# Kernel tuning notes

Measured on AMD Instinct MI355X. Metric: run time of the kernel, lower is better.

## Reference

```python
import jax, jax.numpy as jnp
import numpy as np

EPS = 1e-6
B, N, K = 4, 65536, 16
D_IN, D_OUT, DH = 8, 16, 8  # DH = d_out // 2


def _bn(x, g, b):
    # train-mode BatchNorm2d over (B, N, K) per channel (channels-last here)
    m = jnp.mean(x, axis=(0, 1, 2))
    v = jnp.var(x, axis=(0, 1, 2))
    return (x - m) * jax.lax.rsqrt(v + EPS) * g + b


def _conv(x, w, b):
    # 1x1 Conv2d == per-point linear; x: (B,N,K,Cin), w: (Cout,Cin)
    return jnp.einsum('bnki,oi->bnko', x, w) + b


def _lse(coords, feats, idx, w, b, g, bt):
    # coords: (B,N,3), feats: (B,N,1,D), idx: (B,N,K)
    nbrs = jnp.take_along_axis(coords[:, :, None, :], idx[:, :, :, None], axis=1)  # (B,N,K,3)
    ctr = jnp.broadcast_to(coords[:, :, None, :], nbrs.shape)
    dist = jnp.ones(idx.shape + (1,), dtype=coords.dtype)  # torch path passes idx only -> dist = ones
    enc = jnp.concatenate([ctr, nbrs, ctr - nbrs, dist], axis=-1)  # (B,N,K,10)
    h = jax.nn.relu(_bn(_conv(enc, w, b), g, bt))
    f = jnp.broadcast_to(feats, idx.shape + (feats.shape[-1],))
    return jnp.concatenate([h, f], axis=-1)  # (B,N,K,2*D)


def _pool(x, sw, w, b, g, bt):
    # attentive pooling: softmax over neighbor axis K (axis=2)
    scores = jax.nn.softmax(jnp.einsum('bnki,oi->bnko', x, sw), axis=2)
    agg = jnp.sum(scores * x, axis=2, keepdims=True)  # (B,N,1,C)
    return jax.nn.relu(_bn(_conv(agg, w, b), g, bt))


def setup_inputs() -> dict:
    key = jax.random.key(0)
    ks = jax.random.split(key, 16)
    rn = lambda k, s: (0.1 * jax.random.normal(k, s)).astype(jnp.float32)
    inp = {
        'coords': jax.random.normal(ks[0], (B, N, 3), dtype=jnp.float32),
        'features': jax.random.normal(ks[1], (B, D_IN, N, 1), dtype=jnp.float32),
        'idx': jax.random.randint(ks[2], (B, N, K), 0, N, dtype=jnp.int32),
        # mlp1: d_in -> d_out//2, no bn, LeakyReLU(0.2)
        'w1': rn(ks[3], (DH, D_IN)), 'b1': jnp.zeros((DH,), jnp.float32),
        # lse1 mlp: 10 -> d_out//2, bn + ReLU
        'lse1_w': rn(ks[4], (DH, 10)), 'lse1_b': jnp.zeros((DH,), jnp.float32),
        'lse1_g': jnp.ones((DH,), jnp.float32), 'lse1_bt': jnp.zeros((DH,), jnp.float32),
        # pool1: in d_out -> out d_out//2
        'p1_sw': rn(ks[5], (D_OUT, D_OUT)),
        'p1_w': rn(ks[6], (DH, D_OUT)), 'p1_b': jnp.zeros((DH,), jnp.float32),
        'p1_g': jnp.ones((DH,), jnp.float32), 'p1_bt': jnp.zeros((DH,), jnp.float32),
        # lse2
        'lse2_w': rn(ks[7], (DH, 10)), 'lse2_b': jnp.zeros((DH,), jnp.float32),
        'lse2_g': jnp.ones((DH,), jnp.float32), 'lse2_bt': jnp.zeros((DH,), jnp.float32),
        # pool2: in d_out -> out d_out
        'p2_sw': rn(ks[8], (D_OUT, D_OUT)),
        'p2_w': rn(ks[9], (D_OUT, D_OUT)), 'p2_b': jnp.zeros((D_OUT,), jnp.float32),
        'p2_g': jnp.ones((D_OUT,), jnp.float32), 'p2_bt': jnp.zeros((D_OUT,), jnp.float32),
        # mlp2: d_out -> 2*d_out (no bn/act)
        'w2': rn(ks[10], (2 * D_OUT, D_OUT)), 'b2': jnp.zeros((2 * D_OUT,), jnp.float32),
        # shortcut: d_in -> 2*d_out, bn, no act
        'sc_w': rn(ks[11], (2 * D_OUT, D_IN)), 'sc_b': jnp.zeros((2 * D_OUT,), jnp.float32),
        'sc_g': jnp.ones((2 * D_OUT,), jnp.float32), 'sc_bt': jnp.zeros((2 * D_OUT,), jnp.float32),
    }
    return inp


def reference(coords, features, idx, w1, b1, lse1_w, lse1_b, lse1_g, lse1_bt,
              p1_sw, p1_w, p1_b, p1_g, p1_bt, lse2_w, lse2_b, lse2_g, lse2_bt,
              p2_sw, p2_w, p2_b, p2_g, p2_bt, w2, b2, sc_w, sc_b, sc_g, sc_bt):
    feats = jnp.transpose(features, (0, 2, 3, 1))  # (B,N,1,d_in) channels-last
    x = jax.nn.leaky_relu(_conv(feats, w1, b1), 0.2)           # (B,N,1,DH)
    x = _lse(coords, x, idx, lse1_w, lse1_b, lse1_g, lse1_bt)  # (B,N,K,D_OUT)
    x = _pool(x, p1_sw, p1_w, p1_b, p1_g, p1_bt)               # (B,N,1,DH)
    x = _lse(coords, x, idx, lse2_w, lse2_b, lse2_g, lse2_bt)  # (B,N,K,D_OUT)
    x = _pool(x, p2_sw, p2_w, p2_b, p2_g, p2_bt)               # (B,N,1,D_OUT)
    out = jax.nn.leaky_relu(
        _conv(x, w2, b2) + _bn(_conv(feats, sc_w, sc_b), sc_g, sc_bt), 0.01)
    return jnp.transpose(out, (0, 3, 1, 2))  # (B, 2*d_out, N, 1)
```

## Files before the change

kernel.cpp:

```cpp
#include <hip/hip_runtime.h>

#define NB 4
#define NN 65536
#define NK 16
#define NP (NB * NN)
#define BN_EPS 1e-6f

#define WS_ENC_M   0
#define WS_SC_M    32
#define WS_S_Y2    96
#define WS_SS_Y2   104
#define WS_S_Y4    112
#define WS_SS_Y4   128
#define WS_BN1_SC  160
#define WS_BN1_SH  168
#define WS_BN3_SC  176
#define WS_BN3_SH  184
#define WS_BNSC_SC 192
#define WS_BNSC_SH 224
#define WS_BNP1_SC 256
#define WS_BNP1_SH 264
#define WS_BNP2_SC 272
#define WS_BNP2_SH 288
#define WS_Y2      1024
#define WS_Y4      (1024 + NP * 8)

template <int NCH>
__device__ inline void blockReduceAtomic(float (&v)[NCH], float* __restrict__ dst) {
    __shared__ float red[4][NCH];
    const int lane = threadIdx.x & 63;
    const int wv = threadIdx.x >> 6;
#pragma unroll
    for (int c = 0; c < NCH; c++) {
        float x = v[c];
#pragma unroll
        for (int off = 32; off > 0; off >>= 1) x += __shfl_xor(x, off, 64);
        if (lane == 0) red[wv][c] = x;
    }
    __syncthreads();
    for (int c = threadIdx.x; c < NCH; c += 256)
        atomicAdd(dst + c, red[0][c] + red[1][c] + red[2][c] + red[3][c]);
}

__global__ __launch_bounds__(256) void k_stats1(
    const float* __restrict__ coords, const float* __restrict__ feats,
    const int* __restrict__ idx, float* __restrict__ ws) {
    const int tid = threadIdx.x;
    const int p = blockIdx.x * 256 + tid;
    const int b = p >> 16;
    const int n = p & (NN - 1);

    {
        float accf[44];
        float f[8];
#pragma unroll
        for (int i = 0; i < 8; i++) f[i] = feats[(b * 8 + i) * NN + n];
#pragma unroll
        for (int i = 0; i < 8; i++) accf[i] = f[i];
        int t2 = 8;
#pragma unroll
        for (int i = 0; i < 8; i++)
#pragma unroll
            for (int j = i; j < 8; j++) accf[t2++] = f[i] * f[j];
        blockReduceAtomic<44>(accf, ws + WS_SC_M);
    }

    const float cx = coords[3 * p], cy = coords[3 * p + 1], cz = coords[3 * p + 2];
    const float* cb = coords + b * NN * 3;
    const int4* ip = (const int4*)idx + p * 4;
    float sn0 = 0.f, sn1 = 0.f, sn2 = 0.f;
    float m00 = 0.f, m01 = 0.f, m02 = 0.f, m11 = 0.f, m12 = 0.f, m22 = 0.f;
#pragma unroll
    for (int q = 0; q < 4; q++) {
        int4 v = ip[q];
        int jj[4] = {v.x, v.y, v.z, v.w};
#pragma unroll
        for (int e = 0; e < 4; e++) {
            const int j = jj[e];
            const float nx = cb[3 * j], ny = cb[3 * j + 1], nz = cb[3 * j + 2];
            sn0 += nx; sn1 += ny; sn2 += nz;
            m00 += nx * nx; m01 += nx * ny; m02 += nx * nz;
            m11 += ny * ny; m12 += ny * nz; m22 += nz * nz;
        }
    }
    float acc[27];
    acc[0] = 16.f * cx; acc[1] = 16.f * cy; acc[2] = 16.f * cz;
    acc[3] = sn0; acc[4] = sn1; acc[5] = sn2;
    acc[6] = 16.f * cx * cx; acc[7] = 16.f * cx * cy; acc[8] = 16.f * cx * cz;
    acc[9] = 16.f * cy * cy; acc[10] = 16.f * cy * cz; acc[11] = 16.f * cz * cz;
    acc[12] = cx * sn0; acc[13] = cx * sn1; acc[14] = cx * sn2;
    acc[15] = cy * sn0; acc[16] = cy * sn1; acc[17] = cy * sn2;
    acc[18] = cz * sn0; acc[19] = cz * sn1; acc[20] = cz * sn2;
    acc[21] = m00; acc[22] = m01; acc[23] = m02;
    acc[24] = m11; acc[25] = m12; acc[26] = m22;
    blockReduceAtomic<27>(acc, ws + WS_ENC_M);
}

__global__ void k_fin1(
    const float* __restrict__ lse1_w, const float* __restrict__ lse1_b,
    const float* __restrict__ g1, const float* __restrict__ bt1,
    const float* __restrict__ lse2_w, const float* __restrict__ lse2_b,
    const float* __restrict__ g3, const float* __restrict__ bt3,
    const float* __restrict__ sc_w, const float* __restrict__ sc_b,
    const float* __restrict__ gsc, const float* __restrict__ btsc,
    float* __restrict__ ws) {
    const int t = threadIdx.x;
    if (t < 16) {
        const int c = t & 7;
        const float* w = (t < 8 ? lse1_w : lse2_w) + c * 10;
        const float bb = (t < 8 ? lse1_b : lse2_b)[c];
        float u[6];
        u[0] = w[0] + w[6]; u[1] = w[1] + w[7]; u[2] = w[2] + w[8];
        u[3] = w[3] - w[6]; u[4] = w[4] - w[7]; u[5] = w[5] - w[8];
        const float beta = bb + w[9];
        const float* M = ws + WS_ENC_M;
        float lin = 0.f;
#pragma unroll
        for (int i = 0; i < 6; i++) lin += u[i] * M[i];
        float quad = u[0] * u[0] * M[6] + 2.f * u[0] * u[1] * M[7] + 2.f * u[0] * u[2] * M[8]
                   + u[1] * u[1] * M[9] + 2.f * u[1] * u[2] * M[10] + u[2] * u[2] * M[11];
#pragma unroll
        for (int i = 0; i < 3; i++)
#pragma unroll
            for (int j = 0; j < 3; j++) quad += 2.f * u[i] * u[3 + j] * M[12 + i * 3 + j];
        quad += u[3] * u[3] * M[21] + 2.f * u[3] * u[4] * M[22] + 2.f * u[3] * u[5] * M[23]
              + u[4] * u[4] * M[24] + 2.f * u[4] * u[5] * M[25] + u[5] * u[5] * M[26];
        const float cnt = (float)NP * (float)NK;
        const float sum = lin + cnt * beta;
        const float ss = quad + 2.f * beta * lin + cnt * beta * beta;
        const float m = sum / cnt, v = ss / cnt - m * m;
        const float g = (t < 8 ? g1 : g3)[c], bt = (t < 8 ? bt1 : bt3)[c];
        const float sc = g * rsqrtf(v + BN_EPS);
        if (t < 8) { ws[WS_BN1_SC + c] = sc; ws[WS_BN1_SH + c] = bt - m * sc; }
        else       { ws[WS_BN3_SC + c] = sc; ws[WS_BN3_SH + c] = bt - m * sc; }
    } else if (t < 48) {
        const int c = t - 16;
        const float* w = sc_w + c * 8;
        const float* S = ws + WS_SC_M;
        float lin = 0.f;
#pragma unroll
        for (int i = 0; i < 8; i++) lin += w[i] * S[i];
        float quad = 0.f;
        int t2 = 0;
#pragma unroll
        for (int i = 0; i < 8; i++)
#pragma unroll
            for (int j = i; j < 8; j++) {
                const float mm = S[8 + t2++];
                quad += (i == j ? 1.f : 2.f) * w[i] * w[j] * mm;
            }
        const float cnt = (float)NP;
        const float bb = sc_b[c];
        const float sum = lin + cnt * bb;
        const float ss = quad + 2.f * bb * lin + cnt * bb * bb;
        const float m = sum / cnt, v = ss / cnt - m * m;
        const float sc = gsc[c] * rsqrtf(v + BN_EPS);
        ws[WS_BNSC_SC + c] = sc; ws[WS_BNSC_SH + c] = btsc[c] - m * sc;
    }
}

__global__ __launch_bounds__(256) void k_pool1(
    const float* __restrict__ coords, const float* __restrict__ feats,
    const int* __restrict__ idx,
    const float* __restrict__ w1, const float* __restrict__ b1,
    const float* __restrict__ lse1_w, const float* __restrict__ lse1_b,
    const float* __restrict__ p1_sw, const float* __restrict__ p1_w,
    const float* __restrict__ p1_b, float* __restrict__ ws) {
    __shared__ float lws[80], lbs[8], w1s[64], b1s[8], bnsc[8], bnsh[8],
        sws[64], pws[128], pbs[8];
    const int tid = threadIdx.x;
    for (int i = tid; i < 80; i += 256) lws[i] = lse1_w[i];
    if (tid < 8) {
        lbs[tid] = lse1_b[tid]; b1s[tid] = b1[tid]; pbs[tid] = p1_b[tid];
        bnsc[tid] = ws[WS_BN1_SC + tid]; bnsh[tid] = ws[WS_BN1_SH + tid];
    }
    if (tid < 64) {
        w1s[tid] = w1[tid];
        int o = tid >> 3, i2 = tid & 7;
        sws[tid] = p1_sw[o * 16 + i2];
    }
    if (tid < 128) pws[tid] = p1_w[tid];
    __syncthreads();

    float st[16] = {};
    const int p = blockIdx.x * 256 + tid;
    if (p < NP) {
        const int b = p >> 16;
        const int n = p & (NN - 1);
        float f[8];
#pragma unroll
        for (int i = 0; i < 8; i++) f[i] = feats[(b * 8 + i) * NN + n];
        float x1[8];
#pragma unroll
        for (int j = 0; j < 8; j++) {
            float y = b1s[j];
#pragma unroll
            for (int i = 0; i < 8; i++) y += f[i] * w1s[j * 8 + i];
            x1[j] = y > 0.f ? y : 0.2f * y;
        }
        const float cx = coords[3 * p], cy = coords[3 * p + 1], cz = coords[3 * p + 2];
        const float* cb = coords + b * NN * 3;
        const int4* ip = (const int4*)idx + p * 4;
        int nb[16];
#pragma unroll
        for (int q = 0; q < 4; q++) {
            int4 v = ip[q];
            nb[4 * q] = v.x; nb[4 * q + 1] = v.y; nb[4 * q + 2] = v.z; nb[4 * q + 3] = v.w;
        }
        float l[8] = {}, ac[8] = {};
#pragma unroll
        for (int k = 0; k < 16; k++) {
            const int j = nb[k];
            const float nx = cb[3 * j], ny = cb[3 * j + 1], nz = cb[3 * j + 2];
            const float e6 = cx - nx, e7 = cy - ny, e8 = cz - nz;
            float h[8];
#pragma unroll
            for (int c = 0; c < 8; c++) {
                const float* w = &lws[c * 10];
                float y = lbs[c] + w[9] + cx * w[0] + cy * w[1] + cz * w[2] +
                          nx * w[3] + ny * w[4] + nz * w[5] + e6 * w[6] + e7 * w[7] + e8 * w[8];
                y = y * bnsc[c] + bnsh[c];
                h[c] = y > 0.f ? y : 0.f;
            }
#pragma unroll
            for (int o = 0; o < 8; o++) {
                float s = 0.f;
#pragma unroll
                for (int i = 0; i < 8; i++) s += h[i] * sws[o * 8 + i];
                float e = __expf(s);
                l[o] += e; ac[o] += e * h[o];
            }
        }
        float agg[16];
#pragma unroll
        for (int o = 0; o < 8; o++) agg[o] = ac[o] / l[o];
#pragma unroll
        for (int o = 0; o < 8; o++) agg[8 + o] = x1[o];
#pragma unroll
        for (int c = 0; c < 8; c++) {
            float y = pbs[c];
#pragma unroll
            for (int o = 0; o < 16; o++) y += agg[o] * pws[c * 16 + o];
            ws[WS_Y2 + c * NP + p] = y;
            st[c] = y; st[8 + c] = y * y;
        }
    }
    blockReduceAtomic<16>(st, ws + WS_S_Y2);
}

__global__ void k_fin2(const float* __restrict__ g, const float* __restrict__ bt,
                       float* __restrict__ ws) {
    const int t = threadIdx.x;
    if (t < 8) {
        const float cP = 1.f / (float)NP;
        float m = ws[WS_S_Y2 + t] * cP, v = ws[WS_SS_Y2 + t] * cP - m * m;
        float sc = g[t] * rsqrtf(v + BN_EPS);
        ws[WS_BNP1_SC + t] = sc; ws[WS_BNP1_SH + t] = bt[t] - m * sc;
    }
}

__global__ __launch_bounds__(256) void k_pool2(
    const float* __restrict__ coords, const int* __restrict__ idx,
    const float* __restrict__ lse2_w, const float* __restrict__ lse2_b,
    const float* __restrict__ p2_sw, const float* __restrict__ p2_w,
    const float* __restrict__ p2_b, float* __restrict__ ws) {
    __shared__ float lws[80], lbs[8], bnsc[8], bnsh[8], p1sc[8], p1sh[8],
        sws[64], pws[256], pbs[16];
    const int tid = threadIdx.x;
    for (int i = tid; i < 80; i += 256) lws[i] = lse2_w[i];
    if (tid < 8) {
        lbs[tid] = lse2_b[tid];
        bnsc[tid] = ws[WS_BN3_SC + tid]; bnsh[tid] = ws[WS_BN3_SH + tid];
        p1sc[tid] = ws[WS_BNP1_SC + tid]; p1sh[tid] = ws[WS_BNP1_SH + tid];
    }
    if (tid < 64) {
        int o = tid >> 3, i2 = tid & 7;
        sws[tid] = p2_sw[o * 16 + i2];
    }
    if (tid < 256) pws[tid] = p2_w[tid];
    if (tid < 16) pbs[tid] = p2_b[tid];
    __syncthreads();

    float st[32] = {};
    const int p = blockIdx.x * 256 + tid;
    if (p < NP) {
        const int b = p >> 16;
        float x2[8];
#pragma unroll
        for (int c = 0; c < 8; c++) {
            float y = ws[WS_Y2 + c * NP + p] * p1sc[c] + p1sh[c];
            x2[c] = y > 0.f ? y : 0.f;
        }
        const float cx = coords[3 * p], cy = coords[3 * p + 1], cz = coords[3 * p + 2];
        const float* cb = coords + b * NN * 3;
        const int4* ip = (const int4*)idx + p * 4;
        int nb[16];
#pragma unroll
        for (int q = 0; q < 4; q++) {
            int4 v = ip[q];
            nb[4 * q] = v.x; nb[4 * q + 1] = v.y; nb[4 * q + 2] = v.z; nb[4 * q + 3] = v.w;
        }
        float l[8] = {}, ac[8] = {};
#pragma unroll
        for (int k = 0; k < 16; k++) {
            const int j = nb[k];
            const float nx = cb[3 * j], ny = cb[3 * j + 1], nz = cb[3 * j + 2];
            const float e6 = cx - nx, e7 = cy - ny, e8 = cz - nz;
            float h[8];
#pragma unroll
            for (int c = 0; c < 8; c++) {
                const float* w = &lws[c * 10];
                float y = lbs[c] + w[9] + cx * w[0] + cy * w[1] + cz * w[2] +
                          nx * w[3] + ny * w[4] + nz * w[5] + e6 * w[6] + e7 * w[7] + e8 * w[8];
                y = y * bnsc[c] + bnsh[c];
                h[c] = y > 0.f ? y : 0.f;
            }
#pragma unroll
            for (int o = 0; o < 8; o++) {
                float s = 0.f;
#pragma unroll
                for (int i = 0; i < 8; i++) s += h[i] * sws[o * 8 + i];
                float e = __expf(s);
                l[o] += e; ac[o] += e * h[o];
            }
        }
        float agg[16];
#pragma unroll
        for (int o = 0; o < 8; o++) agg[o] = ac[o] / l[o];
#pragma unroll
        for (int o = 0; o < 8; o++) agg[8 + o] = x2[o];
#pragma unroll
        for (int c = 0; c < 16; c++) {
            float y = pbs[c];
#pragma unroll
            for (int o = 0; o < 16; o++) y += agg[o] * pws[c * 16 + o];
            ws[WS_Y4 + c * NP + p] = y;
            st[c] = y; st[16 + c] = y * y;
        }
    }
    blockReduceAtomic<32>(st, ws + WS_S_Y4);
}

__global__ void k_fin3(const float* __restrict__ g, const float* __restrict__ bt,
                       float* __restrict__ ws) {
    const int t = threadIdx.x;
    if (t < 16) {
        const float cP = 1.f / (float)NP;
        float m = ws[WS_S_Y4 + t] * cP, v = ws[WS_SS_Y4 + t] * cP - m * m;
        float sc = g[t] * rsqrtf(v + BN_EPS);
        ws[WS_BNP2_SC + t] = sc; ws[WS_BNP2_SH + t] = bt[t] - m * sc;
    }
}

__global__ __launch_bounds__(256) void k_final(
    const float* __restrict__ feats, const float* __restrict__ w2,
    const float* __restrict__ b2, const float* __restrict__ sc_w,
    const float* __restrict__ sc_b, const float* __restrict__ ws,
    float* __restrict__ out) {
    __shared__ float w2s[512], b2s[32], scws[256], scbs[32],
        p2sc[16], p2sh[16], scsc[32], scsh[32];
    const int tid = threadIdx.x;
    for (int i = tid; i < 512; i += 256) w2s[i] = w2[i];
    if (tid < 256) scws[tid] = sc_w[tid];
    if (tid < 32) {
        b2s[tid] = b2[tid]; scbs[tid] = sc_b[tid];
        scsc[tid] = ws[WS_BNSC_SC + tid]; scsh[tid] = ws[WS_BNSC_SH + tid];
    }
    if (tid < 16) { p2sc[tid] = ws[WS_BNP2_SC + tid]; p2sh[tid] = ws[WS_BNP2_SH + tid]; }
    __syncthreads();

    const int p = blockIdx.x * 256 + tid;
    if (p >= NP) return;
    const int b = p >> 16;
    const int n = p & (NN - 1);
    float x4[16];
#pragma unroll
    for (int c = 0; c < 16; c++) {
        float y = ws[WS_Y4 + c * NP + p] * p2sc[c] + p2sh[c];
        x4[c] = y > 0.f ? y : 0.f;
    }
    float f[8];
#pragma unroll
    for (int i = 0; i < 8; i++) f[i] = feats[(b * 8 + i) * NN + n];
#pragma unroll
    for (int c = 0; c < 32; c++) {
        float s = scbs[c];
#pragma unroll
        for (int i = 0; i < 8; i++) s += f[i] * scws[c * 8 + i];
        s = s * scsc[c] + scsh[c];
        float m = b2s[c];
#pragma unroll
        for (int o = 0; o < 16; o++) m += x4[o] * w2s[c * 16 + o];
        float v = m + s;
        out[(b * 32 + c) * NN + n] = v > 0.f ? v : 0.01f * v;
    }
}

extern "C" void kernel_launch(void* const* d_in, const int* in_sizes, int n_in,
                              void* d_out, int out_size, void* d_ws, size_t ws_size,
                              hipStream_t stream) {
    (void)in_sizes; (void)n_in; (void)out_size; (void)ws_size;
    const float* coords = (const float*)d_in[0];
    const float* features = (const float*)d_in[1];
    const int* idx = (const int*)d_in[2];
    const float* w1 = (const float*)d_in[3];
    const float* b1 = (const float*)d_in[4];
    const float* lse1_w = (const float*)d_in[5];
    const float* lse1_b = (const float*)d_in[6];
    const float* lse1_g = (const float*)d_in[7];
    const float* lse1_bt = (const float*)d_in[8];
    const float* p1_sw = (const float*)d_in[9];
    const float* p1_w = (const float*)d_in[10];
    const float* p1_b = (const float*)d_in[11];
    const float* p1_g = (const float*)d_in[12];
    const float* p1_bt = (const float*)d_in[13];
    const float* lse2_w = (const float*)d_in[14];
    const float* lse2_b = (const float*)d_in[15];
    const float* lse2_g = (const float*)d_in[16];
    const float* lse2_bt = (const float*)d_in[17];
    const float* p2_sw = (const float*)d_in[18];
    const float* p2_w = (const float*)d_in[19];
    const float* p2_b = (const float*)d_in[20];
    const float* p2_g = (const float*)d_in[21];
    const float* p2_bt = (const float*)d_in[22];
    const float* w2 = (const float*)d_in[23];
    const float* b2 = (const float*)d_in[24];
    const float* sc_w = (const float*)d_in[25];
    const float* sc_b = (const float*)d_in[26];
    const float* sc_g = (const float*)d_in[27];
    const float* sc_bt = (const float*)d_in[28];
    float* ws = (float*)d_ws;
    float* out = (float*)d_out;

    hipMemsetAsync(ws, 0, 144 * sizeof(float), stream);
    k_stats1<<<NP / 256, 256, 0, stream>>>(coords, features, idx, ws);
    k_fin1<<<1, 64, 0, stream>>>(lse1_w, lse1_b, lse1_g, lse1_bt,
                                 lse2_w, lse2_b, lse2_g, lse2_bt,
                                 sc_w, sc_b, sc_g, sc_bt, ws);
    k_pool1<<<NP / 256, 256, 0, stream>>>(coords, features, idx, w1, b1, lse1_w,
                                          lse1_b, p1_sw, p1_w, p1_b, ws);
    k_fin2<<<1, 64, 0, stream>>>(p1_g, p1_bt, ws);
    k_pool2<<<NP / 256, 256, 0, stream>>>(coords, idx, lse2_w, lse2_b, p2_sw,
                                          p2_w, p2_b, ws);
    k_fin3<<<1, 64, 0, stream>>>(p2_g, p2_bt, ws);
    k_final<<<NP / 256, 256, 0, stream>>>(features, w2, b2, sc_w, sc_b, ws, out);
}
```

Measured before the change: 352.9 us.

## Pad coords to float4 scratch, fold BN finalize kernels into consumers, precompute LSE affine

Adds a prep pass that repacks coords into a float4 array, stored temporarily in the output buffer, so each neighbor gather is one 16-byte load instead of three scalar loads. The three single-block finalize kernels are removed; each consumer kernel now computes its BN scale and shift in its prologue, which cuts launches and serialization points. The LSE conv and BN are folded into per-channel affine coefficients split into a center term and a neighbor term, so the per-neighbor math drops to 3 FMAs per channel. Occupancy hints are added to the pool kernels. Reusing the output buffer as scratch relies on k_final overwriting it afterward.

After: 640.9 us. +81.6%, slower.

```diff
diff --git a/kernel.cpp b/kernel.cpp
--- a/kernel.cpp
+++ b/kernel.cpp
@@ -12,16 +12,6 @@
 #define WS_SS_Y2   104
 #define WS_S_Y4    112
 #define WS_SS_Y4   128
-#define WS_BN1_SC  160
-#define WS_BN1_SH  168
-#define WS_BN3_SC  176
-#define WS_BN3_SH  184
-#define WS_BNSC_SC 192
-#define WS_BNSC_SH 224
-#define WS_BNP1_SC 256
-#define WS_BNP1_SH 264
-#define WS_BNP2_SC 272
-#define WS_BNP2_SH 288
 #define WS_Y2      1024
 #define WS_Y4      (1024 + NP * 8)
 
@@ -42,31 +32,59 @@
         atomicAdd(dst + c, red[0][c] + red[1][c] + red[2][c] + red[3][c]);
 }
 
-__global__ __launch_bounds__(256) void k_stats1(
+__device__ inline void bn_from_enc(const float* __restrict__ M, const float* __restrict__ w,
+                                   float b, float g, float bt, float& sc, float& sh) {
+    float u[6];
+    u[0] = w[0] + w[6]; u[1] = w[1] + w[7]; u[2] = w[2] + w[8];
+    u[3] = w[3] - w[6]; u[4] = w[4] - w[7]; u[5] = w[5] - w[8];
+    const float beta = b + w[9];
+    float lin = 0.f;
+#pragma unroll
+    for (int i = 0; i < 6; i++) lin += u[i] * M[i];
+    float quad = u[0] * u[0] * M[6] + 2.f * u[0] * u[1] * M[7] + 2.f * u[0] * u[2] * M[8]
+               + u[1] * u[1] * M[9] + 2.f * u[1] * u[2] * M[10] + u[2] * u[2] * M[11];
+#pragma unroll
+    for (int i = 0; i < 3; i++)
+#pragma unroll
+        for (int j = 0; j < 3; j++) quad += 2.f * u[i] * u[3 + j] * M[12 + i * 3 + j];
+    quad += u[3] * u[3] * M[21] + 2.f * u[3] * u[4] * M[22] + 2.f * u[3] * u[5] * M[23]
+          + u[4] * u[4] * M[24] + 2.f * u[4] * u[5] * M[25] + u[5] * u[5] * M[26];
+    const float cnt = (float)NP * (float)NK;
+    const float sum = lin + cnt * beta;
+    const float ss = quad + 2.f * beta * lin + cnt * beta * beta;
+    const float m = sum / cnt, v = ss / cnt - m * m;
+    sc = g * rsqrtf(v + BN_EPS);
+    sh = bt - m * sc;
+}
+
+__global__ __launch_bounds__(256) void k_prep(
     const float* __restrict__ coords, const float* __restrict__ feats,
-    const int* __restrict__ idx, float* __restrict__ ws) {
+    float4* __restrict__ c4, float* __restrict__ ws) {
     const int tid = threadIdx.x;
     const int p = blockIdx.x * 256 + tid;
     const int b = p >> 16;
     const int n = p & (NN - 1);
-
-    {
-        float accf[44];
-        float f[8];
-#pragma unroll
-        for (int i = 0; i < 8; i++) f[i] = feats[(b * 8 + i) * NN + n];
-#pragma unroll
-        for (int i = 0; i < 8; i++) accf[i] = f[i];
-        int t2 = 8;
-#pragma unroll
-        for (int i = 0; i < 8; i++)
-#pragma unroll
-            for (int j = i; j < 8; j++) accf[t2++] = f[i] * f[j];
-        blockReduceAtomic<44>(accf, ws + WS_SC_M);
-    }
-
-    const float cx = coords[3 * p], cy = coords[3 * p + 1], cz = coords[3 * p + 2];
-    const float* cb = coords + b * NN * 3;
+    c4[p] = make_float4(coords[3 * p], coords[3 * p + 1], coords[3 * p + 2], 0.f);
+    float accf[44];
+    float f[8];
+#pragma unroll
+    for (int i = 0; i < 8; i++) f[i] = feats[(b * 8 + i) * NN + n];
+#pragma unroll
+    for (int i = 0; i < 8; i++) accf[i] = f[i];
+    int t2 = 8;
+#pragma unroll
+    for (int i = 0; i < 8; i++)
+#pragma unroll
+        for (int j = i; j < 8; j++) accf[t2++] = f[i] * f[j];
+    blockReduceAtomic<44>(accf, ws + WS_SC_M);
+}
+
+__global__ __launch_bounds__(256) void k_stats(
+    const float4* __restrict__ c4, const int* __restrict__ idx, float* __restrict__ ws) {
+    const int tid = threadIdx.x;
+    const int p = blockIdx.x * 256 + tid;
+    const int boff = (p >> 16) << 16;
+    const float4 me = c4[p];
     const int4* ip = (const int4*)idx + p * 4;
     float sn0 = 0.f, sn1 = 0.f, sn2 = 0.f;
     float m00 = 0.f, m01 = 0.f, m02 = 0.f, m11 = 0.f, m12 = 0.f, m22 = 0.f;
@@ -76,65 +94,214 @@
         int jj[4] = {v.x, v.y, v.z, v.w};
 #pragma unroll
         for (int e = 0; e < 4; e++) {
-            const int j = jj[e];
-            const float nx = cb[3 * j], ny = cb[3 * j + 1], nz = cb[3 * j + 2];
-            sn0 += nx; sn1 += ny; sn2 += nz;
-            m00 += nx * nx; m01 += nx * ny; m02 += nx * nz;
-            m11 += ny * ny; m12 += ny * nz; m22 += nz * nz;
+            const float4 nn = c4[boff + jj[e]];
+            sn0 += nn.x; sn1 += nn.y; sn2 += nn.z;
+            m00 += nn.x * nn.x; m01 += nn.x * nn.y; m02 += nn.x * nn.z;
+            m11 += nn.y * nn.y; m12 += nn.y * nn.z; m22 += nn.z * nn.z;
         }
     }
     float acc[27];
-    acc[0] = 16.f * cx; acc[1] = 16.f * cy; acc[2] = 16.f * cz;
+    acc[0] = 16.f * me.x; acc[1] = 16.f * me.y; acc[2] = 16.f * me.z;
     acc[3] = sn0; acc[4] = sn1; acc[5] = sn2;
-    acc[6] = 16.f * cx * cx; acc[7] = 16.f * cx * cy; acc[8] = 16.f * cx * cz;
-    acc[9] = 16.f * cy * cy; acc[10] = 16.f * cy * cz; acc[11] = 16.f * cz * cz;
-    acc[12] = cx * sn0; acc[13] = cx * sn1; acc[14] = cx * sn2;
-    acc[15] = cy * sn0; acc[16] = cy * sn1; acc[17] = cy * sn2;
-    acc[18] = cz * sn0; acc[19] = cz * sn1; acc[20] = cz * sn2;
+    acc[6] = 16.f * me.x * me.x; acc[7] = 16.f * me.x * me.y; acc[8] = 16.f * me.x * me.z;
+    acc[9] = 16.f * me.y * me.y; acc[10] = 16.f * me.y * me.z; acc[11] = 16.f * me.z * me.z;
+    acc[12] = me.x * sn0; acc[13] = me.x * sn1; acc[14] = me.x * sn2;
+    acc[15] = me.y * sn0; acc[16] = me.y * sn1; acc[17] = me.y * sn2;
+    acc[18] = me.z * sn0; acc[19] = me.z * sn1; acc[20] = me.z * sn2;
     acc[21] = m00; acc[22] = m01; acc[23] = m02;
     acc[24] = m11; acc[25] = m12; acc[26] = m22;
     blockReduceAtomic<27>(acc, ws + WS_ENC_M);
 }
 
-__global__ void k_fin1(
+__global__ __launch_bounds__(256, 4) void k_pool1(
+    const float4* __restrict__ c4, const float* __restrict__ feats,
+    const int* __restrict__ idx,
+    const float* __restrict__ w1, const float* __restrict__ b1,
     const float* __restrict__ lse1_w, const float* __restrict__ lse1_b,
-    const float* __restrict__ g1, const float* __restrict__ bt1,
+    const float* __restrict__ lse1_g, const float* __restrict__ lse1_bt,
+    const float* __restrict__ p1_sw, const float* __restrict__ p1_w,
+    const float* __restrict__ p1_b, float* __restrict__ ws) {
+    __shared__ float an[24], dc3[24], dcon[8], sws[64], pws[128], pbs[8], w1s[64], b1s[8];
+    const int tid = threadIdx.x;
+    if (tid < 8) {
+        const int c = tid;
+        const float* w = lse1_w + c * 10;
+        float sc, sh;
+        bn_from_enc(ws + WS_ENC_M, w, lse1_b[c], lse1_g[c], lse1_bt[c], sc, sh);
+#pragma unroll
+        for (int i = 0; i < 3; i++) {
+            an[c * 3 + i] = sc * (w[3 + i] - w[6 + i]);
+            dc3[c * 3 + i] = sc * (w[i] + w[6 + i]);
+        }
+        dcon[c] = sc * (lse1_b[c] + w[9]) + sh;
+        b1s[c] = b1[c]; pbs[c] = p1_b[c];
+    }
+    if (tid < 64) {
+        w1s[tid] = w1[tid];
+        sws[tid] = p1_sw[(tid >> 3) * 16 + (tid & 7)];
+    }
+    if (tid < 128) pws[tid] = p1_w[tid];
+    __syncthreads();
+
+    const int p = blockIdx.x * 256 + tid;
+    const int b = p >> 16;
+    const int n = p & (NN - 1);
+    const int boff = b << 16;
+    const float4 me = c4[p];
+    float d[8];
+#pragma unroll
+    for (int c = 0; c < 8; c++)
+        d[c] = dc3[c * 3] * me.x + dc3[c * 3 + 1] * me.y + dc3[c * 3 + 2] * me.z + dcon[c];
+    const int4* ip = (const int4*)idx + p * 4;
+    float l[8] = {}, ac[8] = {};
+#pragma unroll
+    for (int q = 0; q < 4; q++) {
+        int4 v = ip[q];
+        int jj[4] = {v.x, v.y, v.z, v.w};
+#pragma unroll
+        for (int e = 0; e < 4; e++) {
+            const float4 nn = c4[boff + jj[e]];
+            float h[8];
+#pragma unroll
+            for (int c = 0; c < 8; c++) {
+                float y = an[c * 3] * nn.x + an[c * 3 + 1] * nn.y + an[c * 3 + 2] * nn.z + d[c];
+                h[c] = y > 0.f ? y : 0.f;
+            }
+#pragma unroll
+            for (int o = 0; o < 8; o++) {
+                float s = 0.f;
+#pragma unroll
+                for (int i = 0; i < 8; i++) s += h[i] * sws[o * 8 + i];
+                float e2 = __expf(s);
+                l[o] += e2; ac[o] += e2 * h[o];
+            }
+        }
+    }
+    float f[8];
+#pragma unroll
+    for (int i = 0; i < 8; i++) f[i] = feats[(b * 8 + i) * NN + n];
+    float agg[16];
+#pragma unroll
+    for (int o = 0; o < 8; o++) agg[o] = ac[o] / l[o];
+#pragma unroll
+    for (int j = 0; j < 8; j++) {
+        float y = b1s[j];
+#pragma unroll
+        for (int i = 0; i < 8; i++) y += f[i] * w1s[j * 8 + i];
+        agg[8 + j] = y > 0.f ? y : 0.2f * y;
+    }
+    float st[16];
+#pragma unroll
+    for (int c = 0; c < 8; c++) {
+        float y = pbs[c];
+#pragma unroll
+        for (int o = 0; o < 16; o++) y += agg[o] * pws[c * 16 + o];
+        ws[WS_Y2 + c * NP + p] = y;
+        st[c] = y; st[8 + c] = y * y;
+    }
+    blockReduceAtomic<16>(st, ws + WS_S_Y2);
+}
+
+__global__ __launch_bounds__(256, 4) void k_pool2(
+    const float4* __restrict__ c4, const int* __restrict__ idx,
     const float* __restrict__ lse2_w, const float* __restrict__ lse2_b,
-    const float* __restrict__ g3, const float* __restrict__ bt3,
-    const float* __restrict__ sc_w, const float* __restrict__ sc_b,
-    const float* __restrict__ gsc, const float* __restrict__ btsc,
-    float* __restrict__ ws) {
-    const int t = threadIdx.x;
-    if (t < 16) {
-        const int c = t & 7;
-        const float* w = (t < 8 ? lse1_w : lse2_w) + c * 10;
-        const float bb = (t < 8 ? lse1_b : lse2_b)[c];
-        float u[6];
-        u[0] = w[0] + w[6]; u[1] = w[1] + w[7]; u[2] = w[2] + w[8];
-        u[3] = w[3] - w[6]; u[4] = w[4] - w[7]; u[5] = w[5] - w[8];
-        const float beta = bb + w[9];
-        const float* M = ws + WS_ENC_M;
-        float lin = 0.f;
-#pragma unroll
-        for (int i = 0; i < 6; i++) lin += u[i] * M[i];
-        float quad = u[0] * u[0] * M[6] + 2.f * u[0] * u[1] * M[7] + 2.f * u[0] * u[2] * M[8]
-                   + u[1] * u[1] * M[9] + 2.f * u[1] * u[2] * M[10] + u[2] * u[2] * M[11];
-#pragma unroll
-        for (int i = 0; i < 3; i++)
-#pragma unroll
-            for (int j = 0; j < 3; j++) quad += 2.f * u[i] * u[3 + j] * M[12 + i * 3 + j];
-        quad += u[3] * u[3] * M[21] + 2.f * u[3] * u[4] * M[22] + 2.f * u[3] * u[5] * M[23]
-              + u[4] * u[4] * M[24] + 2.f * u[4] * u[5] * M[25] + u[5] * u[5] * M[26];
-        const float cnt = (float)NP * (float)NK;
-        const float sum = lin + cnt * beta;
-        const float ss = quad + 2.f * beta * lin + cnt * beta * beta;
-        const float m = sum / cnt, v = ss / cnt - m * m;
-        const float g = (t < 8 ? g1 : g3)[c], bt = (t < 8 ? bt1 : bt3)[c];
-        const float sc = g * rsqrtf(v + BN_EPS);
-        if (t < 8) { ws[WS_BN1_SC + c] = sc; ws[WS_BN1_SH + c] = bt - m * sc; }
-        else       { ws[WS_BN3_SC + c] = sc; ws[WS_BN3_SH + c] = bt - m * sc; }
-    } else if (t < 48) {
-        const int c = t - 16;
+    const float* __restrict__ lse2_g, const float* __restrict__ lse2_bt,
+    const float* __restrict__ p1_g, const float* __restrict__ p1_bt,
+    const float* __restrict__ p2_sw, const float* __restrict__ p2_w,
+    const float* __restrict__ p2_b, float* __restrict__ ws) {
+    __shared__ float an[24], dc3[24], dcon[8], p1sc[8], p1sh[8],
+        sws[64], pws[256], pbs[16];
+    const int tid = threadIdx.x;
+    if (tid < 8) {
+        const int c = tid;
+        const float* w = lse2_w + c * 10;
+        float sc, sh;
+        bn_from_enc(ws + WS_ENC_M, w, lse2_b[c], lse2_g[c], lse2_bt[c], sc, sh);
+#pragma unroll
+        for (int i = 0; i < 3; i++) {
+            an[c * 3 + i] = sc * (w[3 + i] - w[6 + i]);
+            dc3[c * 3 + i] = sc * (w[i] + w[6 + i]);
+        }
+        dcon[c] = sc * (lse2_b[c] + w[9]) + sh;
+    } else if (tid < 16) {
+        const int c = tid - 8;
+        const float cP = 1.f / (float)NP;
+        float m = ws[WS_S_Y2 + c] * cP, v = ws[WS_SS_Y2 + c] * cP - m * m;
+        float sc = p1_g[c] * rsqrtf(v + BN_EPS);
+        p1sc[c] = sc; p1sh[c] = p1_bt[c] - m * sc;
+    }
+    if (tid < 64) sws[tid] = p2_sw[(tid >> 3) * 16 + (tid & 7)];
+    if (tid < 256) pws[tid] = p2_w[tid];
+    if (tid < 16) pbs[tid] = p2_b[tid];
+    __syncthreads();
+
+    const int p = blockIdx.x * 256 + tid;
+    const int boff = (p >> 16) << 16;
+    const float4 me = c4[p];
+    float d[8];
+#pragma unroll
+    for (int c = 0; c < 8; c++)
+        d[c] = dc3[c * 3] * me.x + dc3[c * 3 + 1] * me.y + dc3[c * 3 + 2] * me.z + dcon[c];
+    const int4* ip = (const int4*)idx + p * 4;
+    float l[8] = {}, ac[8] = {};
+#pragma unroll
+    for (int q = 0; q < 4; q++) {
+        int4 v = ip[q];
+        int jj[4] = {v.x, v.y, v.z, v.w};
+#pragma unroll
+        for (int e = 0; e < 4; e++) {
+            const float4 nn = c4[boff + jj[e]];
+            float h[8];
+#pragma unroll
+            for (int c = 0; c < 8; c++) {
+                float y = an[c * 3] * nn.x + an[c * 3 + 1] * nn.y + an[c * 3 + 2] * nn.z + d[c];
+                h[c] = y > 0.f ? y : 0.f;
+            }
+#pragma unroll
+            for (int o = 0; o < 8; o++) {
+                float s = 0.f;
+#pragma unroll
+                for (int i = 0; i < 8; i++) s += h[i] * sws[o * 8 + i];
+                float e2 = __expf(s);
+                l[o] += e2; ac[o] += e2 * h[o];
+            }
+        }
+    }
+    float agg[16];
+#pragma unroll
+    for (int o = 0; o < 8; o++) agg[o] = ac[o] / l[o];
+#pragma unroll
+    for (int c = 0; c < 8; c++) {
+        float y = ws[WS_Y2 + c * NP + p] * p1sc[c] + p1sh[c];
+        agg[8 + c] = y > 0.f ? y : 0.f;
+    }
+    float st[32];
+#pragma unroll
+    for (int c = 0; c < 16; c++) {
+        float y = pbs[c];
+#pragma unroll
+        for (int o = 0; o < 16; o++) y += agg[o] * pws[c * 16 + o];
+        ws[WS_Y4 + c * NP + p] = y;
+        st[c] = y; st[16 + c] = y * y;
+    }
+    blockReduceAtomic<32>(st, ws + WS_S_Y4);
+}
+
+__global__ __launch_bounds__(256) void k_final(
+    const float* __restrict__ feats, const float* __restrict__ w2,
+    const float* __restrict__ b2, const float* __restrict__ sc_w,
+    const float* __restrict__ sc_b, const float* __restrict__ p2_g,
+    const float* __restrict__ p2_bt, const float* __restrict__ sc_g,
+    const float* __restrict__ sc_bt, const float* __restrict__ ws,
+    float* __restrict__ out) {
+    __shared__ float w2s[512], b2s[32], scws[256], scbs[32],
+        p2sc[16], p2sh[16], scsc[32], scsh[32];
+    const int tid = threadIdx.x;
+    for (int i = tid; i < 512; i += 256) w2s[i] = w2[i];
+    if (tid < 256) scws[tid] = sc_w[tid];
+    if (tid < 32) {
+        b2s[tid] = b2[tid]; scbs[tid] = sc_b[tid];
+        const int c = tid;
         const float* w = sc_w + c * 8;
         const float* S = ws + WS_SC_M;
         float lin = 0.f;
@@ -154,223 +321,19 @@
         const float sum = lin + cnt * bb;
         const float ss = quad + 2.f * bb * lin + cnt * bb * bb;
         const float m = sum / cnt, v = ss / cnt - m * m;
-        const float sc = gsc[c] * rsqrtf(v + BN_EPS);
-        ws[WS_BNSC_SC + c] = sc; ws[WS_BNSC_SH + c] = btsc[c] - m * sc;
-    }
-}
-
-__global__ __launch_bounds__(256) void k_pool1(
-    const float* __restrict__ coords, const float* __restrict__ feats,
-    const int* __restrict__ idx,
-    const float* __restrict__ w1, const float* __restrict__ b1,
-    const float* __restrict__ lse1_w, const float* __restrict__ lse1_b,
-    const float* __restrict__ p1_sw, const float* __restrict__ p1_w,
-    const float* __restrict__ p1_b, float* __restrict__ ws) {
-    __shared__ float lws[80], lbs[8], w1s[64], b1s[8], bnsc[8], bnsh[8],
-        sws[64], pws[128], pbs[8];
-    const int tid = threadIdx.x;
-    for (int i = tid; i < 80; i += 256) lws[i] = lse1_w[i];
-    if (tid < 8) {
-        lbs[tid] = lse1_b[tid]; b1s[tid] = b1[tid]; pbs[tid] = p1_b[tid];
-        bnsc[tid] = ws[WS_BN1_SC + tid]; bnsh[tid] = ws[WS_BN1_SH + tid];
-    }
-    if (tid < 64) {
-        w1s[tid] = w1[tid];
-        int o = tid >> 3, i2 = tid & 7;
-        sws[tid] = p1_sw[o * 16 + i2];
-    }
-    if (tid < 128) pws[tid] = p1_w[tid];
+        const float sc = sc_g[c] * rsqrtf(v + BN_EPS);
+        scsc[c] = sc; scsh[c] = sc_bt[c] - m * sc;
+    }
+    if (tid < 16) {
+        const int c = tid;
+        const float cP = 1.f / (float)NP;
+        float m = ws[WS_S_Y4 + c] * cP, v = ws[WS_SS_Y4 + c] * cP - m * m;
+        float sc = p2_g[c] * rsqrtf(v + BN_EPS);
+        p2sc[c] = sc; p2sh[c] = p2_bt[c] - m * sc;
+    }
     __syncthreads();
 
-    float st[16] = {};
     const int p = blockIdx.x * 256 + tid;
-    if (p < NP) {
-        const int b = p >> 16;
-        const int n = p & (NN - 1);
-        float f[8];
-#pragma unroll
-        for (int i = 0; i < 8; i++) f[i] = feats[(b * 8 + i) * NN + n];
-        float x1[8];
-#pragma unroll
-        for (int j = 0; j < 8; j++) {
-            float y = b1s[j];
-#pragma unroll
-            for (int i = 0; i < 8; i++) y += f[i] * w1s[j * 8 + i];
-            x1[j] = y > 0.f ? y : 0.2f * y;
-        }
-        const float cx = coords[3 * p], cy = coords[3 * p + 1], cz = coords[3 * p + 2];
-        const float* cb = coords + b * NN * 3;
-        const int4* ip = (const int4*)idx + p * 4;
-        int nb[16];
-#pragma unroll
-        for (int q = 0; q < 4; q++) {
-            int4 v = ip[q];
-            nb[4 * q] = v.x; nb[4 * q + 1] = v.y; nb[4 * q + 2] = v.z; nb[4 * q + 3] = v.w;
-        }
-        float l[8] = {}, ac[8] = {};
-#pragma unroll
-        for (int k = 0; k < 16; k++) {
-            const int j = nb[k];
-            const float nx = cb[3 * j], ny = cb[3 * j + 1], nz = cb[3 * j + 2];
-            const float e6 = cx - nx, e7 = cy - ny, e8 = cz - nz;
-            float h[8];
-#pragma unroll
-            for (int c = 0; c < 8; c++) {
-                const float* w = &lws[c * 10];
-                float y = lbs[c] + w[9] + cx * w[0] + cy * w[1] + cz * w[2] +
-                          nx * w[3] + ny * w[4] + nz * w[5] + e6 * w[6] + e7 * w[7] + e8 * w[8];
-                y = y * bnsc[c] + bnsh[c];
-                h[c] = y > 0.f ? y : 0.f;
-            }
-#pragma unroll
-            for (int o = 0; o < 8; o++) {
-                float s = 0.f;
-#pragma unroll
-                for (int i = 0; i < 8; i++) s += h[i] * sws[o * 8 + i];
-                float e = __expf(s);
-                l[o] += e; ac[o] += e * h[o];
-            }
-        }
-        float agg[16];
-#pragma unroll
-        for (int o = 0; o < 8; o++) agg[o] = ac[o] / l[o];
-#pragma unroll
-        for (int o = 0; o < 8; o++) agg[8 + o] = x1[o];
-#pragma unroll
-        for (int c = 0; c < 8; c++) {
-            float y = pbs[c];
-#pragma unroll
-            for (int o = 0; o < 16; o++) y += agg[o] * pws[c * 16 + o];
-            ws[WS_Y2 + c * NP + p] = y;
-            st[c] = y; st[8 + c] = y * y;
-        }
-    }
-    blockReduceAtomic<16>(st, ws + WS_S_Y2);
-}
-
-__global__ void k_fin2(const float* __restrict__ g, const float* __restrict__ bt,
-                       float* __restrict__ ws) {
-    const int t = threadIdx.x;
-    if (t < 8) {
-        const float cP = 1.f / (float)NP;
-        float m = ws[WS_S_Y2 + t] * cP, v = ws[WS_SS_Y2 + t] * cP - m * m;
-        float sc = g[t] * rsqrtf(v + BN_EPS);
-        ws[WS_BNP1_SC + t] = sc; ws[WS_BNP1_SH + t] = bt[t] - m * sc;
-    }
-}
-
-__global__ __launch_bounds__(256) void k_pool2(
-    const float* __restrict__ coords, const int* __restrict__ idx,
-    const float* __restrict__ lse2_w, const float* __restrict__ lse2_b,
-    const float* __restrict__ p2_sw, const float* __restrict__ p2_w,
-    const float* __restrict__ p2_b, float* __restrict__ ws) {
-    __shared__ float lws[80], lbs[8], bnsc[8], bnsh[8], p1sc[8], p1sh[8],
-        sws[64], pws[256], pbs[16];
-    const int tid = threadIdx.x;
-    for (int i = tid; i < 80; i += 256) lws[i] = lse2_w[i];
-    if (tid < 8) {
-        lbs[tid] = lse2_b[tid];
-        bnsc[tid] = ws[WS_BN3_SC + tid]; bnsh[tid] = ws[WS_BN3_SH + tid];
-        p1sc[tid] = ws[WS_BNP1_SC + tid]; p1sh[tid] = ws[WS_BNP1_SH + tid];
-    }
-    if (tid < 64) {
-        int o = tid >> 3, i2 = tid & 7;
-        sws[tid] = p2_sw[o * 16 + i2];
-    }
-    if (tid < 256) pws[tid] = p2_w[tid];
-    if (tid < 16) pbs[tid] = p2_b[tid];
-    __syncthreads();
-
-    float st[32] = {};
-    const int p = blockIdx.x * 256 + tid;
-    if (p < NP) {
-        const int b = p >> 16;
-        float x2[8];
-#pragma unroll
-        for (int c = 0; c < 8; c++) {
-            float y = ws[WS_Y2 + c * NP + p] * p1sc[c] + p1sh[c];
-            x2[c] = y > 0.f ? y : 0.f;
-        }
-        const float cx = coords[3 * p], cy = coords[3 * p + 1], cz = coords[3 * p + 2];
-        const float* cb = coords + b * NN * 3;
-        const int4* ip = (const int4*)idx + p * 4;
-        int nb[16];
-#pragma unroll
-        for (int q = 0; q < 4; q++) {
-            int4 v = ip[q];
-            nb[4 * q] = v.x; nb[4 * q + 1] = v.y; nb[4 * q + 2] = v.z; nb[4 * q + 3] = v.w;
-        }
-        float l[8] = {}, ac[8] = {};
-#pragma unroll
-        for (int k = 0; k < 16; k++) {
-            const int j = nb[k];
-            const float nx = cb[3 * j], ny = cb[3 * j + 1], nz = cb[3 * j + 2];
-            const float e6 = cx - nx, e7 = cy - ny, e8 = cz - nz;
-            float h[8];
-#pragma unroll
-            for (int c = 0; c < 8; c++) {
-                const float* w = &lws[c * 10];
-                float y = lbs[c] + w[9] + cx * w[0] + cy * w[1] + cz * w[2] +
-                          nx * w[3] + ny * w[4] + nz * w[5] + e6 * w[6] + e7 * w[7] + e8 * w[8];
-                y = y * bnsc[c] + bnsh[c];
-                h[c] = y > 0.f ? y : 0.f;
-            }
-#pragma unroll
-            for (int o = 0; o < 8; o++) {
-                float s = 0.f;
-#pragma unroll
-                for (int i = 0; i < 8; i++) s += h[i] * sws[o * 8 + i];
-                float e = __expf(s);
-                l[o] += e; ac[o] += e * h[o];
-            }
-        }
-        float agg[16];
-#pragma unroll
-        for (int o = 0; o < 8; o++) agg[o] = ac[o] / l[o];
-#pragma unroll
-        for (int o = 0; o < 8; o++) agg[8 + o] = x2[o];
-#pragma unroll
-        for (int c = 0; c < 16; c++) {
-            float y = pbs[c];
-#pragma unroll
-            for (int o = 0; o < 16; o++) y += agg[o] * pws[c * 16 + o];
-            ws[WS_Y4 + c * NP + p] = y;
-            st[c] = y; st[16 + c] = y * y;
-        }
-    }
-    blockReduceAtomic<32>(st, ws + WS_S_Y4);
-}
-
-__global__ void k_fin3(const float* __restrict__ g, const float* __restrict__ bt,
-                       float* __restrict__ ws) {
-    const int t = threadIdx.x;
-    if (t < 16) {
-        const float cP = 1.f / (float)NP;
-        float m = ws[WS_S_Y4 + t] * cP, v = ws[WS_SS_Y4 + t] * cP - m * m;
-        float sc = g[t] * rsqrtf(v + BN_EPS);
-        ws[WS_BNP2_SC + t] = sc; ws[WS_BNP2_SH + t] = bt[t] - m * sc;
-    }
-}
-
-__global__ __launch_bounds__(256) void k_final(
-    const float* __restrict__ feats, const float* __restrict__ w2,
-    const float* __restrict__ b2, const float* __restrict__ sc_w,
-    const float* __restrict__ sc_b, const float* __restrict__ ws,
-    float* __restrict__ out) {
-    __shared__ float w2s[512], b2s[32], scws[256], scbs[32],
-        p2sc[16], p2sh[16], scsc[32], scsh[32];
-    const int tid = threadIdx.x;
-    for (int i = tid; i < 512; i += 256) w2s[i] = w2[i];
-    if (tid < 256) scws[tid] = sc_w[tid];
-    if (tid < 32) {
-        b2s[tid] = b2[tid]; scbs[tid] = sc_b[tid];
-        scsc[tid] = ws[WS_BNSC_SC + tid]; scsh[tid] = ws[WS_BNSC_SH + tid];
-    }
-    if (tid < 16) { p2sc[tid] = ws[WS_BNP2_SC + tid]; p2sh[tid] = ws[WS_BNP2_SH + tid]; }
-    __syncthreads();
-
-    const int p = blockIdx.x * 256 + tid;
-    if (p >= NP) return;
     const int b = p >> 16;
     const int n = p & (NN - 1);
     float x4[16];
@@ -431,17 +394,16 @@
     const float* sc_bt = (const float*)d_in[28];
     float* ws = (float*)d_ws;
     float* out = (float*)d_out;
-
+    float4* c4 = (float4*)d_out;
+
+    const int NBLK = NP / 256;
     hipMemsetAsync(ws, 0, 144 * sizeof(float), stream);
-    k_stats1<<<NP / 256, 256, 0, stream>>>(coords, features, idx, ws);
-    k_fin1<<<1, 64, 0, stream>>>(lse1_w, lse1_b, lse1_g, lse1_bt,
-                                 lse2_w, lse2_b, lse2_g, lse2_bt,
-                                 sc_w, sc_b, sc_g, sc_bt, ws);
-    k_pool1<<<NP / 256, 256, 0, stream>>>(coords, features, idx, w1, b1, lse1_w,
-                                          lse1_b, p1_sw, p1_w, p1_b, ws);
-    k_fin2<<<1, 64, 0, stream>>>(p1_g, p1_bt, ws);
-    k_pool2<<<NP / 256, 256, 0, stream>>>(coords, idx, lse2_w, lse2_b, p2_sw,
-                                          p2_w, p2_b, ws);
-    k_fin3<<<1, 64, 0, stream>>>(p2_g, p2_bt, ws);
-    k_final<<<NP / 256, 256, 0, stream>>>(features, w2, b2, sc_w, sc_b, ws, out);
-}
+    k_prep<<<NBLK, 256, 0, stream>>>(coords, features, c4, ws);
+    k_stats<<<NBLK, 256, 0, stream>>>(c4, idx, ws);
+    k_pool1<<<NBLK, 256, 0, stream>>>(c4, features, idx, w1, b1, lse1_w, lse1_b,
+                                      lse1_g, lse1_bt, p1_sw, p1_w, p1_b, ws);
+    k_pool2<<<NBLK, 256, 0, stream>>>(c4, idx, lse2_w, lse2_b, lse2_g, lse2_bt,
+                                      p1_g, p1_bt, p2_sw, p2_w, p2_b, ws);
+    k_final<<<NBLK, 256, 0, stream>>>(features, w2, b2, sc_w, sc_b, p2_g, p2_bt,
+                                      sc_g, sc_bt, ws, out);
+}
```
